# Kernel optimization log

Hardware: AMD Instinct MI355X
Metric: run time of the kernel (lower is better)

Reference implementation:

```python
import jax, jax.numpy as jnp
import numpy as np

H = 48  # hidden_size


def _lstm_cell(inp, h, c, Wih, Whh, bih, bhh):
    # PyTorch LSTMCell: gates ordered (i, f, g, o)
    gates = inp @ Wih.T + h @ Whh.T + bih + bhh
    i, f, g, o = jnp.split(gates, 4, axis=-1)
    i = jax.nn.sigmoid(i)
    f = jax.nn.sigmoid(f)
    g = jnp.tanh(g)
    o = jax.nn.sigmoid(o)
    c_new = f * c + i * g
    h_new = o * jnp.tanh(c_new)
    return h_new, c_new


def setup_inputs() -> dict:
    key = jax.random.key(0)
    ks = jax.random.split(key, 8)
    B, T = 4096, 512
    s = 0.1
    return {
        "x": jax.random.normal(ks[0], (B, T), dtype=jnp.float32),
        "W_ih0": jax.random.normal(ks[1], (4 * H, 1), dtype=jnp.float32) * s,
        "W_hh0": jax.random.normal(ks[2], (4 * H, H), dtype=jnp.float32) * s,
        "b_ih0": jnp.full((4 * H,), 0.01, dtype=jnp.float32),
        "b_hh0": jnp.full((4 * H,), 0.01, dtype=jnp.float32),
        "W_ih1": jax.random.normal(ks[3], (4 * H, H), dtype=jnp.float32) * s,
        "W_hh1": jax.random.normal(ks[4], (4 * H, H), dtype=jnp.float32) * s,
        "b_ih1": jnp.full((4 * H,), 0.01, dtype=jnp.float32),
        "b_hh1": jnp.full((4 * H,), 0.01, dtype=jnp.float32),
        "W_lin": jax.random.normal(ks[5], (1, H), dtype=jnp.float32) * s,
        "b_lin": jnp.full((1,), 0.01, dtype=jnp.float32),
        "future_pred": 64,
    }


def reference(x, W_ih0, W_hh0, b_ih0, b_hh0, W_ih1, W_hh1, b_ih1, b_hh1,
              W_lin, b_lin, future_pred):
    B = x.shape[0]
    h0 = jnp.zeros((B, H), dtype=jnp.float32)
    c0 = jnp.zeros((B, H), dtype=jnp.float32)
    h1 = jnp.zeros((B, H), dtype=jnp.float32)
    c1 = jnp.zeros((B, H), dtype=jnp.float32)

    def tick(h0, c0, h1, c1, inp):  # inp: [B,1]
        h0, c0 = _lstm_cell(inp, h0, c0, W_ih0, W_hh0, b_ih0, b_hh0)
        h1, c1 = _lstm_cell(h0, h1, c1, W_ih1, W_hh1, b_ih1, b_hh1)
        out = h1 @ W_lin.T + b_lin  # [B,1]
        return h0, c0, h1, c1, out

    # teacher-forced pass over observed sequence
    def step_obs(carry, xt):
        h0, c0, h1, c1 = carry
        h0, c0, h1, c1, out = tick(h0, c0, h1, c1, xt)
        return (h0, c0, h1, c1), out

    xs = jnp.swapaxes(x, 0, 1)[:, :, None]  # [T, B, 1]
    (h0, c0, h1, c1), outs_obs = jax.lax.scan(step_obs, (h0, c0, h1, c1), xs)
    last_out = outs_obs[-1]

    def step_fut(carry, _):
        h0, c0, h1, c1, out = carry
        h0, c0, h1, c1, out = tick(h0, c0, h1, c1, out)
        return (h0, c0, h1, c1, out), out

    _, outs_fut = jax.lax.scan(step_fut, (h0, c0, h1, c1, last_out), None,
                               length=future_pred)

    outs = jnp.concatenate([outs_obs, outs_fut], axis=0)  # [T+F, B, 1]
    return jnp.swapaxes(outs[:, :, 0], 0, 1)  # [B, T+F]
```

## Files before the change

kernel.cpp:

```cpp
#include <hip/hip_runtime.h>

#define T_OBS 512
#define NTILE 3
#define RSTRH 200
#define PSTR  20
#define L2E   1.44269504089f

typedef float    f32x4 __attribute__((ext_vector_type(4)));
typedef _Float16 f16x8 __attribute__((ext_vector_type(8)));

#define MF(A,B,C) __builtin_amdgcn_mfma_f32_16x16x32_f16(A, B, C, 0, 0, 0)

__device__ __forceinline__ float lstm_act(const f32x4 a, float& c) {
    const float Ei = __builtin_amdgcn_exp2f(a[0]);
    const float Ef = __builtin_amdgcn_exp2f(a[1]);
    const float Eg = __builtin_amdgcn_exp2f(a[2]);
    const float Eo = __builtin_amdgcn_exp2f(a[3]);
    const float ui = 1.f + Ei, uf = 1.f + Ef, ug = 1.f + Eg, uo = 1.f + Eo;
    const float r1 = __builtin_amdgcn_rcpf(ui * uf);
    const float ig = r1 * uf;
    const float fg = r1 * ui;
    const float r2 = __builtin_amdgcn_rcpf(ug * uo);
    const float og = r2 * ug;
    const float gg = fmaf(r2 * uo, -2.f, 1.f);
    c = fg * c + ig * gg;
    const float Ec = __builtin_amdgcn_exp2f(2.f * L2E * c);
    const float th = fmaf(__builtin_amdgcn_rcpf(1.f + Ec), -2.f, 1.f);
    return og * th;
}

__global__ __launch_bounds__(512, 1) void lstm2_v5(
    const float* __restrict__ x,
    const float* __restrict__ Wih0, const float* __restrict__ Whh0,
    const float* __restrict__ bih0, const float* __restrict__ bhh0,
    const float* __restrict__ Wih1, const float* __restrict__ Whh1,
    const float* __restrict__ bih1, const float* __restrict__ bhh1,
    const float* __restrict__ Wlin, const float* __restrict__ blin,
    const int* __restrict__ fut,
    float* __restrict__ out)
{
    __shared__ __attribute__((aligned(16))) _Float16 s_h[16 * RSTRH];
    __shared__ __attribute__((aligned(16))) float s_pr[2][16 * PSTR];

    const int tid  = threadIdx.x;
    const int wave = tid >> 6;
    const int lane = tid & 63;
    const int n    = lane & 15;
    const int rg   = lane >> 4;
    const bool isL1 = (wave >= 4);
    const int  w    = wave & 3;

    for (int i = tid; i < 16 * RSTRH; i += 512) s_h[i] = (_Float16)0.f;

    const float sgl = ((n & 3) == 2) ? 2.f * L2E : -L2E;

    f16x8 ah[NTILE][3], al[NTILE][3];
    #pragma unroll
    for (int i = 0; i < NTILE; ++i) {
        const int m  = 3 * w + i;
        const int rp = 16 * m + n;
        const int r0 = (rp & 3) * 48 + (rp >> 2);
        #pragma unroll
        for (int s = 0; s < 3; ++s)
            #pragma unroll
            for (int j = 0; j < 8; ++j) {
                const int k = 32 * s + 8 * rg + j;
                float v;
                if (isL1) v = ((k < 48) ? Wih1[r0 * 48 + k] : Whh1[r0 * 48 + (k - 48)]) * sgl;
                else      v = (s < 2 && k < 48) ? Whh0[r0 * 48 + k] * sgl : 0.f;
                const _Float16 hi = (_Float16)v;
                ah[i][s][j] = hi;
                al[i][s][j] = (_Float16)(v - (float)hi);
            }
    }

    const float sg4[4] = { -L2E, -L2E, 2.f * L2E, -L2E };
    f32x4 bv[NTILE], wi0v[NTILE];
    float wlq[NTILE];
    int   hu[NTILE];
    #pragma unroll
    for (int i = 0; i < NTILE; ++i) {
        const int u = 4 * (3 * w + i) + rg;
        hu[i]  = u;
        wlq[i] = Wlin[u];
        #pragma unroll
        for (int g = 0; g < 4; ++g) {
            bv[i][g]   = (isL1 ? (bih1[g * 48 + u] + bhh1[g * 48 + u])
                               : (bih0[g * 48 + u] + bhh0[g * 48 + u])) * sg4[g];
            wi0v[i][g] = Wih0[g * 48 + u] * sg4[g];
        }
    }

    int koff[3];
    #pragma unroll
    for (int s = 0; s < 3; ++s) {
        const int k0 = 32 * s + 8 * rg;
        koff[s] = (k0 < 48) ? k0 : k0 + 48;
    }

    const int F    = fut[0];
    const int TT   = T_OBS + F;
    const int bb0  = blockIdx.x * 16;
    const float bl = blin[0];
    const int xrow = (bb0 + n) * T_OBS;
    const int nb   = n * RSTRH;
    const int prh  = n * PSTR + w * 4 + rg;

    float cc[NTILE];
    #pragma unroll
    for (int i = 0; i < NTILE; ++i) cc[i] = 0.f;

    const f32x4 z4 = { 0.f, 0.f, 0.f, 0.f };

    __syncthreads();

    if (!isL1) {
        const float x0 = x[xrow];
        #pragma unroll
        for (int i = 0; i < NTILE; ++i) {
            const f32x4 a = bv[i] + wi0v[i] * x0;
            s_h[nb + hu[i]] = (_Float16)lstm_act(a, cc[i]);
        }
    }
    __syncthreads();

    float xcur = 0.f;
    if (!isL1) xcur = x[xrow + 1];

    for (int tau = 1; tau < T_OBS; ++tau) {
        const int cb = (tau & 1) * 48;
        const int pb = 48 - cb;
        const int rb = nb + pb;

        if (!isL1) {
            const float xnxt = x[xrow + ((tau + 1 < T_OBS) ? tau + 1 : T_OBS - 1)];
            if (tau >= 2 && tid < 16) {
                const float* pr = &s_pr[(tau - 1) & 1][tid * PSTR];
                const f32x4 s = *(const f32x4*)(pr) + *(const f32x4*)(pr + 4)
                              + *(const f32x4*)(pr + 8) + *(const f32x4*)(pr + 12);
                out[(bb0 + tid) * TT + (tau - 2)] = s[0] + s[1] + s[2] + s[3] + bl;
            }
            const f16x8 bh0 = *(const f16x8*)(s_h + rb + koff[0]);
            const f16x8 bh1 = *(const f16x8*)(s_h + rb + koff[1]);
            f32x4 Aq[NTILE], Bq[NTILE];
            #pragma unroll
            for (int i = 0; i < NTILE; ++i) {
                Aq[i] = MF(ah[i][0], bh0, bv[i]);
                Aq[i] = MF(al[i][0], bh0, Aq[i]);
                Bq[i] = MF(ah[i][1], bh1, z4);
                Bq[i] = MF(al[i][1], bh1, Bq[i]);
            }
            #pragma unroll
            for (int i = 0; i < NTILE; ++i) {
                const f32x4 a = Aq[i] + Bq[i] + wi0v[i] * xcur;
                s_h[nb + cb + hu[i]] = (_Float16)lstm_act(a, cc[i]);
            }
            xcur = xnxt;
        } else {
            f16x8 bh[3];
            #pragma unroll
            for (int s = 0; s < 3; ++s) bh[s] = *(const f16x8*)(s_h + rb + koff[s]);
            f32x4 Aq[NTILE], Bq[NTILE];
            #pragma unroll
            for (int i = 0; i < NTILE; ++i) {
                Aq[i] = MF(ah[i][0], bh[0], bv[i]);
                Aq[i] = MF(al[i][0], bh[0], Aq[i]);
                Aq[i] = MF(ah[i][1], bh[1], Aq[i]);
                Bq[i] = MF(al[i][1], bh[1], z4);
                Bq[i] = MF(ah[i][2], bh[2], Bq[i]);
                Bq[i] = MF(al[i][2], bh[2], Bq[i]);
            }
            float part = 0.f;
            #pragma unroll
            for (int i = 0; i < NTILE; ++i) {
                const f32x4 a = Aq[i] + Bq[i];
                const float h = lstm_act(a, cc[i]);
                s_h[nb + 96 + cb + hu[i]] = (_Float16)h;
                part = fmaf(h, wlq[i], part);
            }
            s_pr[tau & 1][prh] = part;
        }
        __syncthreads();
    }

    if (tid < 16) {
        const float* pr = &s_pr[1][tid * PSTR];
        const f32x4 s = *(const f32x4*)(pr) + *(const f32x4*)(pr + 4)
                      + *(const f32x4*)(pr + 8) + *(const f32x4*)(pr + 12);
        out[(bb0 + tid) * TT + (T_OBS - 2)] = s[0] + s[1] + s[2] + s[3] + bl;
    }

    for (int tau = T_OBS; tau <= TT; ++tau) {
        const int cb = (tau & 1) * 48;
        const int pb = 48 - cb;
        const int rb = nb + pb;

        f32x4 Aq[NTILE], Bq[NTILE];
        if (isL1) {
            f16x8 bh[3];
            #pragma unroll
            for (int s = 0; s < 3; ++s) bh[s] = *(const f16x8*)(s_h + rb + koff[s]);
            #pragma unroll
            for (int i = 0; i < NTILE; ++i) {
                Aq[i] = MF(ah[i][0], bh[0], bv[i]);
                Aq[i] = MF(al[i][0], bh[0], Aq[i]);
                Aq[i] = MF(ah[i][1], bh[1], Aq[i]);
                Bq[i] = MF(al[i][1], bh[1], z4);
                Bq[i] = MF(ah[i][2], bh[2], Bq[i]);
                Bq[i] = MF(al[i][2], bh[2], Bq[i]);
            }
            float part = 0.f;
            #pragma unroll
            for (int i = 0; i < NTILE; ++i) {
                const f32x4 a = Aq[i] + Bq[i];
                const float h = lstm_act(a, cc[i]);
                s_h[nb + 96 + cb + hu[i]] = (_Float16)h;
                part = fmaf(h, wlq[i], part);
            }
            s_pr[tau & 1][prh] = part;
        } else {
            const f16x8 bh0 = *(const f16x8*)(s_h + rb + koff[0]);
            const f16x8 bh1 = *(const f16x8*)(s_h + rb + koff[1]);
            #pragma unroll
            for (int i = 0; i < NTILE; ++i) {
                Aq[i] = MF(ah[i][0], bh0, bv[i]);
                Aq[i] = MF(al[i][0], bh0, Aq[i]);
                Bq[i] = MF(ah[i][1], bh1, z4);
                Bq[i] = MF(al[i][1], bh1, Bq[i]);
            }
        }
        __syncthreads();

        if (!isL1) {
            const float* pr = &s_pr[tau & 1][n * PSTR];
            const f32x4 s = *(const f32x4*)(pr) + *(const f32x4*)(pr + 4)
                          + *(const f32x4*)(pr + 8) + *(const f32x4*)(pr + 12);
            const float o = s[0] + s[1] + s[2] + s[3] + bl;
            if (tid < 16) out[(bb0 + n) * TT + (tau - 1)] = o;
            if (tau < TT) {
                #pragma unroll
                for (int i = 0; i < NTILE; ++i) {
                    const f32x4 a = Aq[i] + Bq[i] + wi0v[i] * o;
                    s_h[nb + cb + hu[i]] = (_Float16)lstm_act(a, cc[i]);
                }
            }
        }
        __syncthreads();
    }
}

extern "C" void kernel_launch(void* const* d_in, const int* in_sizes, int n_in,
                              void* d_out, int out_size, void* d_ws, size_t ws_size,
                              hipStream_t stream) {
    const float* x    = (const float*)d_in[0];
    const float* Wih0 = (const float*)d_in[1];
    const float* Whh0 = (const float*)d_in[2];
    const float* bih0 = (const float*)d_in[3];
    const float* bhh0 = (const float*)d_in[4];
    const float* Wih1 = (const float*)d_in[5];
    const float* Whh1 = (const float*)d_in[6];
    const float* bih1 = (const float*)d_in[7];
    const float* bhh1 = (const float*)d_in[8];
    const float* Wlin = (const float*)d_in[9];
    const float* blin = (const float*)d_in[10];
    const int*   fut  = (const int*)d_in[11];
    float* out = (float*)d_out;

    const int B    = in_sizes[0] / T_OBS;
    const int grid = B / 16;
    lstm2_v5<<<grid, 512, 0, stream>>>(
        x, Wih0, Whh0, bih0, bhh0, Wih1, Whh1, bih1, bhh1, Wlin, blin, fut, out);
}
```

Measured before the change: 540.2 us.

## Spread LSTM gate tiles over 12 waves and unroll steady loop by two

Raises the block from 8 to 12 waves (6 per layer), so each wave handles 2 gate tiles instead of 3. This shortens each wave's serial MFMA and activation chain per timestep. The partial-sum stride and reduction grow to cover 24 entries. The observed-sequence loop is also unrolled by two with constant ping-pong offsets, which removes the per-step index arithmetic. In exchange there are more waves per block-wide barrier and more partial sums to reduce per step.

Measured after the change: 544.3 us. About the same (+0.7%).

```diff
diff --git a/kernel.cpp b/kernel.cpp
--- a/kernel.cpp
+++ b/kernel.cpp
@@ -1,9 +1,10 @@
 #include <hip/hip_runtime.h>
 
 #define T_OBS 512
-#define NTILE 3
+#define NTILE 2
+#define NWAVE 12
 #define RSTRH 200
-#define PSTR  20
+#define PSTR  28
 #define L2E   1.44269504089f
 
 typedef float    f32x4 __attribute__((ext_vector_type(4)));
@@ -29,7 +30,7 @@
     return og * th;
 }
 
-__global__ __launch_bounds__(512, 1) void lstm2_v5(
+__global__ __launch_bounds__(768, 1) void lstm2_v6(
     const float* __restrict__ x,
     const float* __restrict__ Wih0, const float* __restrict__ Whh0,
     const float* __restrict__ bih0, const float* __restrict__ bhh0,
@@ -47,17 +48,17 @@
     const int lane = tid & 63;
     const int n    = lane & 15;
     const int rg   = lane >> 4;
-    const bool isL1 = (wave >= 4);
-    const int  w    = wave & 3;
-
-    for (int i = tid; i < 16 * RSTRH; i += 512) s_h[i] = (_Float16)0.f;
+    const bool isL1 = (wave >= 6);
+    const int  w    = isL1 ? (wave - 6) : wave;
+
+    for (int i = tid; i < 16 * RSTRH; i += 768) s_h[i] = (_Float16)0.f;
 
     const float sgl = ((n & 3) == 2) ? 2.f * L2E : -L2E;
 
     f16x8 ah[NTILE][3], al[NTILE][3];
     #pragma unroll
     for (int i = 0; i < NTILE; ++i) {
-        const int m  = 3 * w + i;
+        const int m  = NTILE * w + i;
         const int rp = 16 * m + n;
         const int r0 = (rp & 3) * 48 + (rp >> 2);
         #pragma unroll
@@ -80,7 +81,7 @@
     int   hu[NTILE];
     #pragma unroll
     for (int i = 0; i < NTILE; ++i) {
-        const int u = 4 * (3 * w + i) + rg;
+        const int u = 4 * (NTILE * w + i) + rg;
         hu[i]  = u;
         wlq[i] = Wlin[u];
         #pragma unroll
@@ -127,40 +128,83 @@
     float xcur = 0.f;
     if (!isL1) xcur = x[xrow + 1];
 
-    for (int tau = 1; tau < T_OBS; ++tau) {
+#define STEADY(TAU_, CB_, PB_) do {                                              \
+    if (!isL1) {                                                                 \
+        const float xnxt = x[xrow + (((TAU_) + 1 < T_OBS) ? (TAU_) + 1 : T_OBS - 1)]; \
+        if ((TAU_) >= 2 && tid < 16) {                                           \
+            const float* pr = &s_pr[((TAU_) - 1) & 1][tid * PSTR];               \
+            const f32x4 sv = *(const f32x4*)(pr)      + *(const f32x4*)(pr + 4)  \
+                           + *(const f32x4*)(pr + 8)  + *(const f32x4*)(pr + 12) \
+                           + *(const f32x4*)(pr + 16) + *(const f32x4*)(pr + 20);\
+            out[(bb0 + tid) * TT + ((TAU_) - 2)] = sv[0]+sv[1]+sv[2]+sv[3]+bl;   \
+        }                                                                        \
+        const f16x8 bh0 = *(const f16x8*)(s_h + nb + (PB_) + koff[0]);           \
+        const f16x8 bh1 = *(const f16x8*)(s_h + nb + (PB_) + koff[1]);           \
+        f32x4 Aq[NTILE], Bq[NTILE];                                              \
+        _Pragma("unroll")                                                        \
+        for (int i = 0; i < NTILE; ++i) {                                        \
+            Aq[i] = MF(ah[i][0], bh0, bv[i]);                                    \
+            Aq[i] = MF(al[i][0], bh0, Aq[i]);                                    \
+            Bq[i] = MF(ah[i][1], bh1, z4);                                       \
+            Bq[i] = MF(al[i][1], bh1, Bq[i]);                                    \
+        }                                                                        \
+        _Pragma("unroll")                                                        \
+        for (int i = 0; i < NTILE; ++i) {                                        \
+            const f32x4 a = Aq[i] + Bq[i] + wi0v[i] * xcur;                      \
+            s_h[nb + (CB_) + hu[i]] = (_Float16)lstm_act(a, cc[i]);              \
+        }                                                                        \
+        xcur = xnxt;                                                             \
+    } else {                                                                     \
+        const f16x8 bh0 = *(const f16x8*)(s_h + nb + (PB_) + koff[0]);           \
+        const f16x8 bh1 = *(const f16x8*)(s_h + nb + (PB_) + koff[1]);           \
+        const f16x8 bh2 = *(const f16x8*)(s_h + nb + (PB_) + koff[2]);           \
+        f32x4 Aq[NTILE], Bq[NTILE];                                              \
+        _Pragma("unroll")                                                        \
+        for (int i = 0; i < NTILE; ++i) {                                        \
+            Aq[i] = MF(ah[i][0], bh0, bv[i]);                                    \
+            Aq[i] = MF(al[i][0], bh0, Aq[i]);                                    \
+            Aq[i] = MF(ah[i][1], bh1, Aq[i]);                                    \
+            Bq[i] = MF(al[i][1], bh1, z4);                                       \
+            Bq[i] = MF(ah[i][2], bh2, Bq[i]);                                    \
+            Bq[i] = MF(al[i][2], bh2, Bq[i]);                                    \
+        }                                                                        \
+        float part = 0.f;                                                        \
+        _Pragma("unroll")                                                        \
+        for (int i = 0; i < NTILE; ++i) {                                        \
+            const f32x4 a = Aq[i] + Bq[i];                                       \
+            const float h = lstm_act(a, cc[i]);                                  \
+            s_h[nb + 96 + (CB_) + hu[i]] = (_Float16)h;                          \
+            part = fmaf(h, wlq[i], part);                                        \
+        }                                                                        \
+        s_pr[(TAU_) & 1][prh] = part;                                            \
+    }                                                                            \
+    __syncthreads();                                                             \
+} while (0)
+
+    for (int tau = 1; tau < T_OBS - 1; tau += 2) {
+        STEADY(tau,     48, 0);
+        STEADY(tau + 1,  0, 48);
+    }
+    STEADY(T_OBS - 1, 48, 0);
+
+    if (tid < 16) {
+        const float* pr = &s_pr[1][tid * PSTR];
+        const f32x4 sv = *(const f32x4*)(pr)      + *(const f32x4*)(pr + 4)
+                       + *(const f32x4*)(pr + 8)  + *(const f32x4*)(pr + 12)
+                       + *(const f32x4*)(pr + 16) + *(const f32x4*)(pr + 20);
+        out[(bb0 + tid) * TT + (T_OBS - 2)] = sv[0] + sv[1] + sv[2] + sv[3] + bl;
+    }
+
+    for (int tau = T_OBS; tau <= TT; ++tau) {
         const int cb = (tau & 1) * 48;
         const int pb = 48 - cb;
         const int rb = nb + pb;
 
-        if (!isL1) {
-            const float xnxt = x[xrow + ((tau + 1 < T_OBS) ? tau + 1 : T_OBS - 1)];
-            if (tau >= 2 && tid < 16) {
-                const float* pr = &s_pr[(tau - 1) & 1][tid * PSTR];
-                const f32x4 s = *(const f32x4*)(pr) + *(const f32x4*)(pr + 4)
-                              + *(const f32x4*)(pr + 8) + *(const f32x4*)(pr + 12);
-                out[(bb0 + tid) * TT + (tau - 2)] = s[0] + s[1] + s[2] + s[3] + bl;
-            }
-            const f16x8 bh0 = *(const f16x8*)(s_h + rb + koff[0]);
-            const f16x8 bh1 = *(const f16x8*)(s_h + rb + koff[1]);
-            f32x4 Aq[NTILE], Bq[NTILE];
-            #pragma unroll
-            for (int i = 0; i < NTILE; ++i) {
-                Aq[i] = MF(ah[i][0], bh0, bv[i]);
-                Aq[i] = MF(al[i][0], bh0, Aq[i]);
-                Bq[i] = MF(ah[i][1], bh1, z4);
-                Bq[i] = MF(al[i][1], bh1, Bq[i]);
-            }
-            #pragma unroll
-            for (int i = 0; i < NTILE; ++i) {
-                const f32x4 a = Aq[i] + Bq[i] + wi0v[i] * xcur;
-                s_h[nb + cb + hu[i]] = (_Float16)lstm_act(a, cc[i]);
-            }
-            xcur = xnxt;
-        } else {
+        f32x4 Aq[NTILE], Bq[NTILE];
+        if (isL1) {
             f16x8 bh[3];
             #pragma unroll
             for (int s = 0; s < 3; ++s) bh[s] = *(const f16x8*)(s_h + rb + koff[s]);
-            f32x4 Aq[NTILE], Bq[NTILE];
             #pragma unroll
             for (int i = 0; i < NTILE; ++i) {
                 Aq[i] = MF(ah[i][0], bh[0], bv[i]);
@@ -179,45 +223,6 @@
                 part = fmaf(h, wlq[i], part);
             }
             s_pr[tau & 1][prh] = part;
-        }
-        __syncthreads();
-    }
-
-    if (tid < 16) {
-        const float* pr = &s_pr[1][tid * PSTR];
-        const f32x4 s = *(const f32x4*)(pr) + *(const f32x4*)(pr + 4)
-                      + *(const f32x4*)(pr + 8) + *(const f32x4*)(pr + 12);
-        out[(bb0 + tid) * TT + (T_OBS - 2)] = s[0] + s[1] + s[2] + s[3] + bl;
-    }
-
-    for (int tau = T_OBS; tau <= TT; ++tau) {
-        const int cb = (tau & 1) * 48;
-        const int pb = 48 - cb;
-        const int rb = nb + pb;
-
-        f32x4 Aq[NTILE], Bq[NTILE];
-        if (isL1) {
-            f16x8 bh[3];
-            #pragma unroll
-            for (int s = 0; s < 3; ++s) bh[s] = *(const f16x8*)(s_h + rb + koff[s]);
-            #pragma unroll
-            for (int i = 0; i < NTILE; ++i) {
-                Aq[i] = MF(ah[i][0], bh[0], bv[i]);
-                Aq[i] = MF(al[i][0], bh[0], Aq[i]);
-                Aq[i] = MF(ah[i][1], bh[1], Aq[i]);
-                Bq[i] = MF(al[i][1], bh[1], z4);
-                Bq[i] = MF(ah[i][2], bh[2], Bq[i]);
-                Bq[i] = MF(al[i][2], bh[2], Bq[i]);
-            }
-            float part = 0.f;
-            #pragma unroll
-            for (int i = 0; i < NTILE; ++i) {
-                const f32x4 a = Aq[i] + Bq[i];
-                const float h = lstm_act(a, cc[i]);
-                s_h[nb + 96 + cb + hu[i]] = (_Float16)h;
-                part = fmaf(h, wlq[i], part);
-            }
-            s_pr[tau & 1][prh] = part;
         } else {
             const f16x8 bh0 = *(const f16x8*)(s_h + rb + koff[0]);
             const f16x8 bh1 = *(const f16x8*)(s_h + rb + koff[1]);
@@ -233,9 +238,10 @@
 
         if (!isL1) {
             const float* pr = &s_pr[tau & 1][n * PSTR];
-            const f32x4 s = *(const f32x4*)(pr) + *(const f32x4*)(pr + 4)
-                          + *(const f32x4*)(pr + 8) + *(const f32x4*)(pr + 12);
-            const float o = s[0] + s[1] + s[2] + s[3] + bl;
+            const f32x4 sv = *(const f32x4*)(pr)      + *(const f32x4*)(pr + 4)
+                           + *(const f32x4*)(pr + 8)  + *(const f32x4*)(pr + 12)
+                           + *(const f32x4*)(pr + 16) + *(const f32x4*)(pr + 20);
+            const float o = sv[0] + sv[1] + sv[2] + sv[3] + bl;
             if (tid < 16) out[(bb0 + n) * TT + (tau - 1)] = o;
             if (tau < TT) {
                 #pragma unroll
@@ -268,6 +274,6 @@
 
     const int B    = in_sizes[0] / T_OBS;
     const int grid = B / 16;
-    lstm2_v5<<<grid, 512, 0, stream>>>(
+    lstm2_v6<<<grid, 768, 0, stream>>>(
         x, Wih0, Whh0, bih0, bhh0, Wih1, Whh1, bih1, bhh1, Wlin, blin, fut, out);
 }
```
